# Kernel tuning notes

Hardware: AMD Instinct MI355X
Metric: run time of the kernel (lower is better)

Reference implementation:

```python
import jax, jax.numpy as jnp
import numpy as np

N = 100000      # nodes
E = 1600000     # edges
G = 1000        # graphs in the batch
D_IN, D_H, D_OUT = 128, 128, 64


def setup_inputs() -> dict:
    key = jax.random.key(0)
    ks = jax.random.split(key, 8)
    x = jax.random.normal(ks[0], (N, D_IN), jnp.float32)
    edge_index = jax.random.randint(ks[1], (2, E), 0, N, dtype=jnp.int32)
    batch = jnp.sort(jax.random.randint(ks[2], (N,), 0, G, dtype=jnp.int32))
    s_in = 1.0 / np.sqrt(D_IN)
    s_h = 1.0 / np.sqrt(D_H)
    return {
        "x": x,
        "edge_index": edge_index,
        "batch": batch,
        "W_emb": jax.random.normal(ks[3], (D_IN, D_H), jnp.float32) * s_in,
        "b_emb": jnp.zeros((D_H,), jnp.float32),
        "W1": jax.random.normal(ks[4], (D_H, D_H), jnp.float32) * s_h,
        "b1": jnp.zeros((D_H,), jnp.float32),
        "W2": jax.random.normal(ks[5], (D_H, D_H), jnp.float32) * s_h,
        "b2": jnp.zeros((D_H,), jnp.float32),
        "W3": jax.random.normal(ks[6], (D_H, D_OUT), jnp.float32) * s_h,
        "b3": jnp.zeros((D_OUT,), jnp.float32),
    }


def reference(x, edge_index, batch, W_emb, b_emb, W1, b1, W2, b2, W3, b3):
    # Eval mode: dropout is identity.
    n = x.shape[0]
    src, dst = edge_index[0], edge_index[1]
    # GCN symmetric normalization with self-loops (Kipf & Welling).
    deg = jax.ops.segment_sum(jnp.ones(src.shape[0], x.dtype), dst, num_segments=n) + 1.0
    dis = jax.lax.rsqrt(deg)                 # deg^{-1/2}, [N]
    edge_norm = dis[src] * dis[dst]          # [E]
    self_norm = dis * dis                    # self-loop weight = 1/deg, [N]

    def gcn_conv(h, W, b):
        h = h @ W                                         # [N, d_out]
        agg = jax.ops.segment_sum(h[src] * edge_norm[:, None], dst, num_segments=n)
        return agg + h * self_norm[:, None] + b

    h = x @ W_emb + b_emb
    h = jax.nn.relu(gcn_conv(h, W1, b1))
    h = jax.nn.relu(gcn_conv(h, W2, b2))
    h = gcn_conv(h, W3, b3)
    # global_add_pool over graph ids
    return jax.ops.segment_sum(h, batch, num_segments=G)
```

## Files before the change

### kernel.cpp

```cpp
#include <hip/hip_runtime.h>
#include <hip/hip_bf16.h>

#define NN 100000
#define NE 1600000
#define NG 1000
#define SMAX 48

typedef unsigned short u16;
typedef unsigned int u32;
typedef u16 u16x8 __attribute__((ext_vector_type(8)));
typedef u32 u32x4 __attribute__((ext_vector_type(4)));
typedef float f32x4 __attribute__((ext_vector_type(4)));
typedef __attribute__((ext_vector_type(8))) short s16x8;
typedef __attribute__((ext_vector_type(4))) float facc4;

__device__ __forceinline__ float bf2f(u16 u) {
    union { u32 i; float f; } c; c.i = ((u32)u) << 16; return c.f;
}
__device__ __forceinline__ u16 f2bf(float f) {
    __hip_bfloat16 h = __float2bfloat16(f);
    union { __hip_bfloat16 h; u16 u; } c; c.h = h; return c.u;
}

__global__ __launch_bounds__(256) void detect_kernel(const u32* __restrict__ xr, int* __restrict__ flag) {
    __shared__ int cnt[256];
    int c = 0;
    for (int i = threadIdx.x; i < 4096; i += 256) {
        u32 e = (xr[i] >> 7) & 0xFFu;
        if (e >= 110u && e <= 135u) c++;
    }
    cnt[threadIdx.x] = c;
    __syncthreads();
    for (int o = 128; o > 0; o >>= 1) {
        if (threadIdx.x < o) cnt[threadIdx.x] += cnt[threadIdx.x + o];
        __syncthreads();
    }
    if (threadIdx.x == 0) flag[0] = (cnt[0] > 2048) ? 1 : 0;
}

#define MEGA_NB 12726
__global__ __launch_bounds__(256) void mega_prep(
    const void* __restrict__ x, const int* __restrict__ flag, u16* __restrict__ xb,
    const void* __restrict__ Wemb, const void* __restrict__ W1, const void* __restrict__ W2,
    const void* __restrict__ W3, u16* __restrict__ wembT, u16* __restrict__ w1T,
    u16* __restrict__ w2T, u16* __restrict__ w3T,
    const void* __restrict__ bemb, const void* __restrict__ b1, const void* __restrict__ b2,
    const void* __restrict__ b3, float* __restrict__ bembF, float* __restrict__ b1F,
    float* __restrict__ b2F, float* __restrict__ b3F,
    const int* __restrict__ ei, int* __restrict__ counts)
{
    int b = blockIdx.x, tid = threadIdx.x;
    int fl = flag[0];
    if (b < 6250) {
        if (fl) return;
        int c = b * 256 + tid;
        f32x4 a = reinterpret_cast<const f32x4*>(x)[c * 2];
        f32x4 d = reinterpret_cast<const f32x4*>(x)[c * 2 + 1];
        u16x8 o;
        #pragma unroll
        for (int j = 0; j < 4; ++j) { o[j] = f2bf(a[j]); o[4 + j] = f2bf(d[j]); }
        reinterpret_cast<u16x8*>(xb)[c] = o;
    } else if (b < 6474) {
        int o = (b - 6250) * 256 + tid;
        const void* src; u16* dst; int M; int ol;
        if (o < 16384)      { src = Wemb; dst = wembT; M = 128; ol = o; }
        else if (o < 32768) { src = W1;   dst = w1T;   M = 128; ol = o - 16384; }
        else if (o < 49152) { src = W2;   dst = w2T;   M = 128; ol = o - 32768; }
        else                { src = W3;   dst = w3T;   M = 64;  ol = o - 49152; }
        int n = ol >> 7, k = ol & 127;
        u16 v = fl ? reinterpret_cast<const u16*>(src)[k * M + n]
                   : f2bf(reinterpret_cast<const float*>(src)[k * M + n]);
        dst[ol] = v;
    } else if (b < 6476) {
        int i = (b - 6474) * 256 + tid;
        if (i >= 448) return;
        const void* src; float* dst; int il;
        if (i < 128)      { src = bemb; dst = bembF; il = i; }
        else if (i < 256) { src = b1;   dst = b1F;   il = i - 128; }
        else if (i < 384) { src = b2;   dst = b2F;   il = i - 256; }
        else              { src = b3;   dst = b3F;   il = i - 384; }
        dst[il] = fl ? bf2f(reinterpret_cast<const u16*>(src)[il])
                     : reinterpret_cast<const float*>(src)[il];
    } else {
        int e = (b - 6476) * 256 + tid;
        if (e < NE) atomicAdd(&counts[ei[NE + e]], 1);
    }
}

__global__ __launch_bounds__(256) void wfuse_kernel(const u16* __restrict__ w1T, const u16* __restrict__ wembT,
                                                    const float* __restrict__ bembF,
                                                    u16* __restrict__ WfT, float* __restrict__ bfW) {
    int b = blockIdx.x;
    if (b < 64) {
        int o = b * 256 + threadIdx.x;
        int n = o >> 7, k = o & 127;
        float acc = 0.f;
        #pragma unroll 4
        for (int j = 0; j < 128; ++j)
            acc += bf2f(w1T[n * 128 + j]) * bf2f(wembT[j * 128 + k]);
        WfT[o] = f2bf(acc);
    } else {
        int n = threadIdx.x;
        if (n < 128) {
            float acc = 0.f;
            for (int j = 0; j < 128; ++j)
                acc += bembF[j] * bf2f(w1T[n * 128 + j]);
            bfW[n] = acc;
        }
    }
}

__global__ __launch_bounds__(256) void scan1_kernel(const int* __restrict__ counts, int* __restrict__ offs,
                                                    int* __restrict__ bsums, float* __restrict__ dis,
                                                    int* __restrict__ cursor) {
    __shared__ int sums[256];
    int tid = threadIdx.x;
    int base = blockIdx.x * 2048 + tid * 8;
    int local[8];
    int s = 0;
    #pragma unroll
    for (int i = 0; i < 8; ++i) {
        int v = 0;
        if (base + i < NN) {
            v = counts[base + i];
            dis[base + i] = rsqrtf((float)v + 1.0f);
            cursor[base + i] = 0;
        }
        local[i] = s; s += v;
    }
    sums[tid] = s;
    __syncthreads();
    for (int o = 1; o < 256; o <<= 1) {
        int v = (tid >= o) ? sums[tid - o] : 0;
        __syncthreads();
        sums[tid] += v;
        __syncthreads();
    }
    int excl = sums[tid] - s;
    #pragma unroll
    for (int i = 0; i < 8; ++i)
        if (base + i < NN) offs[base + i] = excl + local[i];
    if (tid == 255) bsums[blockIdx.x] = sums[255];
}

__global__ __launch_bounds__(256) void scan3_kernel(int* __restrict__ offs, const int* __restrict__ bsums) {
    __shared__ int addv;
    int i = blockIdx.x * 256 + threadIdx.x;
    int bucket = blockIdx.x >> 3;
    if (threadIdx.x == 0) {
        int s = 0;
        for (int k = 0; k < bucket; ++k) s += bsums[k];
        addv = s;
    }
    __syncthreads();
    if (i < NN) offs[i] += addv;
}

__global__ __launch_bounds__(256) void scatter_kernel(const int* __restrict__ ei, const int* __restrict__ offs,
                                                      int* __restrict__ cursor, const float* __restrict__ dis,
                                                      int2* __restrict__ edges) {
    int e = blockIdx.x * 256 + threadIdx.x;
    if (e < NE) {
        int s = ei[e], d = ei[NE + e];
        int pos = offs[d] + atomicAdd(&cursor[d], 1);
        int2 pk;
        pk.x = s;
        pk.y = __float_as_int(dis[s] * dis[d]);
        edges[pos] = pk;
    }
}

__global__ __launch_bounds__(256) void gemm_emb(const u16* __restrict__ xb, const u16* __restrict__ xraw,
                                                const int* __restrict__ flag, const u16* __restrict__ WfT,
                                                const float* __restrict__ bfW, u16* __restrict__ Hout) {
    __shared__ u16 sW[128 * 136];
    int tid = threadIdx.x;
    const u16* A = flag[0] ? xraw : xb;
    for (int c = tid; c < 128 * 16; c += 256) {
        int n = c >> 4, kc = (c & 15) << 3;
        *reinterpret_cast<u16x8*>(sW + n * 136 + kc) = reinterpret_cast<const u16x8*>(WfT)[c];
    }
    __syncthreads();
    int wv = tid >> 6, lane = tid & 63;
    int m = lane & 15, quad = lane >> 4;
    int r0 = blockIdx.x * 64 + wv * 16;
    int ar = r0 + m; if (ar >= NN) ar = NN - 1;
    facc4 acc[8];
    #pragma unroll
    for (int t = 0; t < 8; ++t) acc[t] = (facc4){0.f, 0.f, 0.f, 0.f};
    const u16* arow = A + (size_t)ar * 128 + quad * 8;
    #pragma unroll
    for (int k0 = 0; k0 < 128; k0 += 32) {
        s16x8 a = *reinterpret_cast<const s16x8*>(arow + k0);
        #pragma unroll
        for (int t = 0; t < 8; ++t) {
            s16x8 bfr = *reinterpret_cast<const s16x8*>(sW + (t * 16 + m) * 136 + k0 + quad * 8);
            acc[t] = __builtin_amdgcn_mfma_f32_16x16x32_bf16(a, bfr, acc[t], 0, 0, 0);
        }
    }
    #pragma unroll
    for (int t = 0; t < 8; ++t) {
        int col = t * 16 + m;
        float bv = bfW[col];
        #pragma unroll
        for (int r = 0; r < 4; ++r) {
            int orow = r0 + quad * 4 + r;
            if (orow < NN)
                Hout[(size_t)orow * 128 + col] = f2bf(acc[t][r] + bv);
        }
    }
}

template <int MOUT>
__global__ __launch_bounds__(256) void fused_agg_gemm(const u16* __restrict__ T, const int* __restrict__ offs,
                                                      const int* __restrict__ counts, const float* __restrict__ dis,
                                                      const int2* __restrict__ edges, const float* __restrict__ aggbias,
                                                      const u16* __restrict__ Wt, u16* __restrict__ Hout) {
    constexpr int LDW = 136;
    __shared__ u16 sW[MOUT * LDW];
    __shared__ u16 sA[64 * LDW];
    int tid = threadIdx.x;
    for (int c = tid; c < MOUT * 16; c += 256) {
        int n = c >> 4, kc = (c & 15) << 3;
        *reinterpret_cast<u16x8*>(sW + n * LDW + kc) = reinterpret_cast<const u16x8*>(Wt)[c];
    }

    int lane = tid & 15, grp = tid >> 4;
    const u32x4* T4 = reinterpret_cast<const u32x4*>(T);
    for (int i = 0; i < 4; ++i) {
        int nl = grp * 4 + i;
        int n = blockIdx.x * 64 + nl;
        bool valid = n < NN;
        int nc = valid ? n : NN - 1;
        float di = dis[nc];
        float sn = di * di;
        u32x4 ts = T4[(size_t)nc * 16 + lane];
        float acc[8];
        #pragma unroll
        for (int q = 0; q < 4; ++q) {
            acc[2 * q]     = bf2f((u16)(ts[q] & 0xffffu)) * sn + aggbias[lane * 8 + 2 * q];
            acc[2 * q + 1] = bf2f((u16)(ts[q] >> 16))     * sn + aggbias[lane * 8 + 2 * q + 1];
        }
        int st = offs[nc], cnt = valid ? counts[nc] : 0;
        int j = 0;
        for (; j + 4 <= cnt; j += 4) {
            int2 e0 = edges[st + j];
            int2 e1 = edges[st + j + 1];
            int2 e2 = edges[st + j + 2];
            int2 e3 = edges[st + j + 3];
            u32x4 g0 = T4[(size_t)e0.x * 16 + lane];
            u32x4 g1 = T4[(size_t)e1.x * 16 + lane];
            u32x4 g2 = T4[(size_t)e2.x * 16 + lane];
            u32x4 g3 = T4[(size_t)e3.x * 16 + lane];
            float w0 = __int_as_float(e0.y), w1 = __int_as_float(e1.y);
            float w2 = __int_as_float(e2.y), w3 = __int_as_float(e3.y);
            #pragma unroll
            for (int q = 0; q < 4; ++q) {
                acc[2 * q]     += bf2f((u16)(g0[q] & 0xffffu)) * w0;
                acc[2 * q + 1] += bf2f((u16)(g0[q] >> 16))     * w0;
                acc[2 * q]     += bf2f((u16)(g1[q] & 0xffffu)) * w1;
                acc[2 * q + 1] += bf2f((u16)(g1[q] >> 16))     * w1;
                acc[2 * q]     += bf2f((u16)(g2[q] & 0xffffu)) * w2;
                acc[2 * q + 1] += bf2f((u16)(g2[q] >> 16))     * w2;
                acc[2 * q]     += bf2f((u16)(g3[q] & 0xffffu)) * w3;
                acc[2 * q + 1] += bf2f((u16)(g3[q] >> 16))     * w3;
            }
        }
        for (; j < cnt; ++j) {
            int2 e = edges[st + j];
            u32x4 g = T4[(size_t)e.x * 16 + lane];
            float w = __int_as_float(e.y);
            #pragma unroll
            for (int q = 0; q < 4; ++q) {
                acc[2 * q]     += bf2f((u16)(g[q] & 0xffffu)) * w;
                acc[2 * q + 1] += bf2f((u16)(g[q] >> 16))     * w;
            }
        }
        u16x8 pk;
        #pragma unroll
        for (int q = 0; q < 4; ++q) {
            pk[2 * q]     = f2bf(fmaxf(acc[2 * q], 0.0f));
            pk[2 * q + 1] = f2bf(fmaxf(acc[2 * q + 1], 0.0f));
        }
        *reinterpret_cast<u16x8*>(sA + nl * LDW + lane * 8) = pk;
    }
    __syncthreads();

    int wv = tid >> 6, l64 = tid & 63;
    int m = l64 & 15, quad = l64 >> 4;
    int r0 = blockIdx.x * 64 + wv * 16;
    constexpr int NT = MOUT / 16;
    facc4 gacc[NT];
    #pragma unroll
    for (int t = 0; t < NT; ++t) gacc[t] = (facc4){0.f, 0.f, 0.f, 0.f};
    #pragma unroll
    for (int k0 = 0; k0 < 128; k0 += 32) {
        s16x8 a = *reinterpret_cast<const s16x8*>(sA + (wv * 16 + m) * LDW + k0 + quad * 8);
        #pragma unroll
        for (int t = 0; t < NT; ++t) {
            s16x8 bfr = *reinterpret_cast<const s16x8*>(sW + (t * 16 + m) * LDW + k0 + quad * 8);
            gacc[t] = __builtin_amdgcn_mfma_f32_16x16x32_bf16(a, bfr, gacc[t], 0, 0, 0);
        }
    }
    #pragma unroll
    for (int t = 0; t < NT; ++t) {
        int col = t * 16 + m;
        #pragma unroll
        for (int r = 0; r < 4; ++r) {
            int orow = r0 + quad * 4 + r;
            if (orow < NN)
                Hout[(size_t)orow * MOUT + col] = f2bf(gacc[t][r]);
        }
    }
}

__global__ __launch_bounds__(256) void agg_pool_kernel(const u16* __restrict__ T, const int* __restrict__ offs,
                                                       const int* __restrict__ counts, const float* __restrict__ dis,
                                                       const int2* __restrict__ edges, const float* __restrict__ bias,
                                                       const int* __restrict__ batch, float* __restrict__ outF) {
    __shared__ float accG[SMAX * 64];
    __shared__ int sg0;
    int tid = threadIdx.x;
    for (int i = tid; i < SMAX * 64; i += 256) accG[i] = 0.0f;
    if (tid == 0) sg0 = batch[blockIdx.x * 32];
    __syncthreads();
    int g0 = sg0;
    int lane = tid & 7;
    int n = blockIdx.x * 32 + (tid >> 3);

    const u32x4* T4 = reinterpret_cast<const u32x4*>(T);
    float di = dis[n];
    float sn = di * di;
    u32x4 ts = T4[(size_t)n * 8 + lane];
    float acc[8];
    #pragma unroll
    for (int q = 0; q < 4; ++q) {
        acc[2 * q]     = bf2f((u16)(ts[q] & 0xffffu)) * sn + bias[lane * 8 + 2 * q];
        acc[2 * q + 1] = bf2f((u16)(ts[q] >> 16))     * sn + bias[lane * 8 + 2 * q + 1];
    }
    int st = offs[n], cnt = counts[n];
    int j = 0;
    for (; j + 4 <= cnt; j += 4) {
        int2 e0 = edges[st + j];
        int2 e1 = edges[st + j + 1];
        int2 e2 = edges[st + j + 2];
        int2 e3 = edges[st + j + 3];
        u32x4 g0v = T4[(size_t)e0.x * 8 + lane];
        u32x4 g1v = T4[(size_t)e1.x * 8 + lane];
        u32x4 g2v = T4[(size_t)e2.x * 8 + lane];
        u32x4 g3v = T4[(size_t)e3.x * 8 + lane];
        float w0 = __int_as_float(e0.y), w1 = __int_as_float(e1.y);
        float w2 = __int_as_float(e2.y), w3 = __int_as_float(e3.y);
        #pragma unroll
        for (int q = 0; q < 4; ++q) {
            acc[2 * q]     += bf2f((u16)(g0v[q] & 0xffffu)) * w0;
            acc[2 * q + 1] += bf2f((u16)(g0v[q] >> 16))     * w0;
            acc[2 * q]     += bf2f((u16)(g1v[q] & 0xffffu)) * w1;
            acc[2 * q + 1] += bf2f((u16)(g1v[q] >> 16))     * w1;
            acc[2 * q]     += bf2f((u16)(g2v[q] & 0xffffu)) * w2;
            acc[2 * q + 1] += bf2f((u16)(g2v[q] >> 16))     * w2;
            acc[2 * q]     += bf2f((u16)(g3v[q] & 0xffffu)) * w3;
            acc[2 * q + 1] += bf2f((u16)(g3v[q] >> 16))     * w3;
        }
    }
    for (; j < cnt; ++j) {
        int2 e = edges[st + j];
        u32x4 g = T4[(size_t)e.x * 8 + lane];
        float w = __int_as_float(e.y);
        #pragma unroll
        for (int q = 0; q < 4; ++q) {
            acc[2 * q]     += bf2f((u16)(g[q] & 0xffffu)) * w;
            acc[2 * q + 1] += bf2f((u16)(g[q] >> 16))     * w;
        }
    }

    int s = batch[n] - g0;
    if (s >= 0 && s < SMAX) {
        #pragma unroll
        for (int q = 0; q < 8; ++q)
            atomicAdd(&accG[s * 64 + lane * 8 + q], acc[q]);
    } else {
        #pragma unroll
        for (int q = 0; q < 8; ++q)
            atomicAdd(&outF[(size_t)(g0 + s) * 64 + lane * 8 + q], acc[q]);
    }
    __syncthreads();
    int gend = batch[blockIdx.x * 32 + 31];
    int span = gend - g0 + 1;
    if (span > SMAX) span = SMAX;
    for (int i = tid; i < span * 64; i += 256)
        atomicAdd(&outF[(size_t)g0 * 64 + i], accG[i]);
}

__global__ __launch_bounds__(256) void out_cvt_kernel(const float* __restrict__ outF, void* __restrict__ out,
                                                      const int* __restrict__ flag) {
    int i = blockIdx.x * 256 + threadIdx.x;
    if (i < NG * 64) {
        float v = outF[i];
        if (flag[0]) reinterpret_cast<u16*>(out)[i] = f2bf(v);
        else         reinterpret_cast<float*>(out)[i] = v;
    }
}

extern "C" void kernel_launch(void* const* d_in, const int* in_sizes, int n_in,
                              void* d_out, int out_size, void* d_ws, size_t ws_size,
                              hipStream_t stream) {
    const void* x     = d_in[0];
    const int* ei     = (const int*)d_in[1];
    const int* batch  = (const int*)d_in[2];
    const void* W_emb = d_in[3];
    const void* b_emb = d_in[4];
    const void* W1    = d_in[5];
    const void* b1    = d_in[6];
    const void* W2    = d_in[7];
    const void* b2    = d_in[8];
    const void* W3    = d_in[9];
    const void* b3    = d_in[10];

    char* p = (char*)d_ws;
    auto alloc = [&](size_t bytes) { void* r = p; p += (bytes + 255) & ~(size_t)255; return r; };
    int*   flag   = (int*)alloc(256);
    int*   counts = (int*)alloc(NN * 4);
    int*   cursor = (int*)alloc(NN * 4);
    int*   offs   = (int*)alloc(NN * 4);
    float* dis    = (float*)alloc(NN * 4);
    int*   bsums  = (int*)alloc(256 * 4);
    int2*  edges  = (int2*)alloc((size_t)NE * 8);
    u16*   wembT  = (u16*)alloc(128 * 128 * 2);
    u16*   w1T    = (u16*)alloc(128 * 128 * 2);
    u16*   w2T    = (u16*)alloc(128 * 128 * 2);
    u16*   w3T    = (u16*)alloc(64 * 128 * 2);
    u16*   WfT    = (u16*)alloc(128 * 128 * 2);
    float* bembF  = (float*)alloc(128 * 4);
    float* b1F    = (float*)alloc(128 * 4);
    float* b2F    = (float*)alloc(128 * 4);
    float* b3F    = (float*)alloc(64 * 4);
    float* bfW    = (float*)alloc(128 * 4);
    float* outF   = (float*)alloc((size_t)NG * 64 * 4);
    u16*   hA     = (u16*)alloc((size_t)(NN + 64) * 128 * 2);
    u16*   hB     = (u16*)alloc((size_t)(NN + 64) * 128 * 2);

    hipMemsetAsync(counts, 0, NN * 4, stream);
    hipMemsetAsync(outF, 0, (size_t)NG * 64 * 4, stream);

    const int SB = (NN + 2047) / 2048;
    const int NB = (NN + 255) / 256;
    const int GB = (NN + 63) / 64;
    const int EB = (NE + 255) / 256;

    detect_kernel<<<1, 256, 0, stream>>>((const u32*)x, flag);
    mega_prep<<<MEGA_NB, 256, 0, stream>>>(x, flag, hB, W_emb, W1, W2, W3, wembT, w1T, w2T, w3T,
                                           b_emb, b1, b2, b3, bembF, b1F, b2F, b3F, ei, counts);
    wfuse_kernel<<<65, 256, 0, stream>>>(w1T, wembT, bembF, WfT, bfW);
    scan1_kernel<<<SB, 256, 0, stream>>>(counts, offs, bsums, dis, cursor);
    scan3_kernel<<<NB, 256, 0, stream>>>(offs, bsums);
    scatter_kernel<<<EB, 256, 0, stream>>>(ei, offs, cursor, dis, edges);
    gemm_emb<<<GB, 256, 0, stream>>>(hB, (const u16*)x, flag, WfT, bfW, hA);
    fused_agg_gemm<128><<<GB, 256, 0, stream>>>(hA, offs, counts, dis, edges, b1F, w2T, hB);
    fused_agg_gemm<64><<<GB, 256, 0, stream>>>(hB, offs, counts, dis, edges, b2F, w3T, hA);
    agg_pool_kernel<<<NN / 32, 256, 0, stream>>>(hA, offs, counts, dis, edges, b3F, batch, outF);
    out_cvt_kernel<<<(NG * 64 + 255) / 256, 256, 0, stream>>>(outF, d_out, flag);
}
```

Measured before the change: 515.0 us.

## Record edge rank during counting and aggregate directly into MFMA A-fragments

The degree-counting atomic now stores each edge's rank within its destination bucket. The scatter pass then places edges without a second atomic pass, and the cursor array and its reset go away. The fused aggregation+GEMM kernel is restructured so each lane aggregates the exact features it needs as an MFMA A operand (16 nodes per wave, 4 column chunks per lane). This removes the LDS staging buffer and one round trip through shared memory. In exchange, register pressure rises (32 accumulators plus 8 gathered vectors per lane), the gather unroll drops from 4 to 2 edges, and the rank scratch buffer is aliased onto hA.

```diff
diff --git a/kernel.cpp b/kernel.cpp
--- a/kernel.cpp
+++ b/kernel.cpp
@@ -47,7 +47,7 @@
     const void* __restrict__ bemb, const void* __restrict__ b1, const void* __restrict__ b2,
     const void* __restrict__ b3, float* __restrict__ bembF, float* __restrict__ b1F,
     float* __restrict__ b2F, float* __restrict__ b3F,
-    const int* __restrict__ ei, int* __restrict__ counts)
+    const int* __restrict__ ei, int* __restrict__ counts, int* __restrict__ erank)
 {
     int b = blockIdx.x, tid = threadIdx.x;
     int fl = flag[0];
@@ -83,7 +83,10 @@
                      : reinterpret_cast<const float*>(src)[il];
     } else {
         int e = (b - 6476) * 256 + tid;
-        if (e < NE) atomicAdd(&counts[ei[NE + e]], 1);
+        if (e < NE) {
+            int d = ei[NE + e];
+            erank[e] = atomicAdd(&counts[d], 1);
+        }
     }
 }
 
@@ -111,8 +114,7 @@
 }
 
 __global__ __launch_bounds__(256) void scan1_kernel(const int* __restrict__ counts, int* __restrict__ offs,
-                                                    int* __restrict__ bsums, float* __restrict__ dis,
-                                                    int* __restrict__ cursor) {
+                                                    int* __restrict__ bsums, float* __restrict__ dis) {
     __shared__ int sums[256];
     int tid = threadIdx.x;
     int base = blockIdx.x * 2048 + tid * 8;
@@ -124,7 +126,6 @@
         if (base + i < NN) {
             v = counts[base + i];
             dis[base + i] = rsqrtf((float)v + 1.0f);
-            cursor[base + i] = 0;
         }
         local[i] = s; s += v;
     }
@@ -157,12 +158,12 @@
 }
 
 __global__ __launch_bounds__(256) void scatter_kernel(const int* __restrict__ ei, const int* __restrict__ offs,
-                                                      int* __restrict__ cursor, const float* __restrict__ dis,
+                                                      const int* __restrict__ erank, const float* __restrict__ dis,
                                                       int2* __restrict__ edges) {
     int e = blockIdx.x * 256 + threadIdx.x;
     if (e < NE) {
         int s = ei[e], d = ei[NE + e];
-        int pos = offs[d] + atomicAdd(&cursor[d], 1);
+        int pos = offs[d] + erank[e];
         int2 pk;
         pk.x = s;
         pk.y = __float_as_int(dis[s] * dis[d]);
@@ -218,90 +219,90 @@
                                                       const u16* __restrict__ Wt, u16* __restrict__ Hout) {
     constexpr int LDW = 136;
     __shared__ u16 sW[MOUT * LDW];
-    __shared__ u16 sA[64 * LDW];
     int tid = threadIdx.x;
     for (int c = tid; c < MOUT * 16; c += 256) {
         int n = c >> 4, kc = (c & 15) << 3;
         *reinterpret_cast<u16x8*>(sW + n * LDW + kc) = reinterpret_cast<const u16x8*>(Wt)[c];
     }
 
-    int lane = tid & 15, grp = tid >> 4;
+    int wv = tid >> 6, lane = tid & 63;
+    int m = lane & 15, quad = lane >> 4;
+    int n = blockIdx.x * 64 + wv * 16 + m;
+    bool valid = n < NN;
+    int nc = valid ? n : NN - 1;
     const u32x4* T4 = reinterpret_cast<const u32x4*>(T);
-    for (int i = 0; i < 4; ++i) {
-        int nl = grp * 4 + i;
-        int n = blockIdx.x * 64 + nl;
-        bool valid = n < NN;
-        int nc = valid ? n : NN - 1;
-        float di = dis[nc];
-        float sn = di * di;
-        u32x4 ts = T4[(size_t)nc * 16 + lane];
-        float acc[8];
+
+    float di = dis[nc];
+    float sn = di * di;
+    float acc[4][8];
+    #pragma unroll
+    for (int c = 0; c < 4; ++c) {
+        u32x4 ts = T4[(size_t)nc * 16 + quad + 4 * c];
         #pragma unroll
         for (int q = 0; q < 4; ++q) {
-            acc[2 * q]     = bf2f((u16)(ts[q] & 0xffffu)) * sn + aggbias[lane * 8 + 2 * q];
-            acc[2 * q + 1] = bf2f((u16)(ts[q] >> 16))     * sn + aggbias[lane * 8 + 2 * q + 1];
-        }
-        int st = offs[nc], cnt = valid ? counts[nc] : 0;
-        int j = 0;
-        for (; j + 4 <= cnt; j += 4) {
-            int2 e0 = edges[st + j];
-            int2 e1 = edges[st + j + 1];
-            int2 e2 = edges[st + j + 2];
-            int2 e3 = edges[st + j + 3];
-            u32x4 g0 = T4[(size_t)e0.x * 16 + lane];
-            u32x4 g1 = T4[(size_t)e1.x * 16 + lane];
-            u32x4 g2 = T4[(size_t)e2.x * 16 + lane];
-            u32x4 g3 = T4[(size_t)e3.x * 16 + lane];
-            float w0 = __int_as_float(e0.y), w1 = __int_as_float(e1.y);
-            float w2 = __int_as_float(e2.y), w3 = __int_as_float(e3.y);
+            int f = c * 32 + quad * 8 + 2 * q;
+            acc[c][2 * q]     = bf2f((u16)(ts[q] & 0xffffu)) * sn + aggbias[f];
+            acc[c][2 * q + 1] = bf2f((u16)(ts[q] >> 16))     * sn + aggbias[f + 1];
+        }
+    }
+    int st = offs[nc], cnt = valid ? counts[nc] : 0;
+    int j = 0;
+    for (; j + 2 <= cnt; j += 2) {
+        int2 e0 = edges[st + j];
+        int2 e1 = edges[st + j + 1];
+        u32x4 g0[4], g1[4];
+        #pragma unroll
+        for (int c = 0; c < 4; ++c) g0[c] = T4[(size_t)e0.x * 16 + quad + 4 * c];
+        #pragma unroll
+        for (int c = 0; c < 4; ++c) g1[c] = T4[(size_t)e1.x * 16 + quad + 4 * c];
+        float w0 = __int_as_float(e0.y), w1 = __int_as_float(e1.y);
+        #pragma unroll
+        for (int c = 0; c < 4; ++c)
             #pragma unroll
             for (int q = 0; q < 4; ++q) {
-                acc[2 * q]     += bf2f((u16)(g0[q] & 0xffffu)) * w0;
-                acc[2 * q + 1] += bf2f((u16)(g0[q] >> 16))     * w0;
-                acc[2 * q]     += bf2f((u16)(g1[q] & 0xffffu)) * w1;
-                acc[2 * q + 1] += bf2f((u16)(g1[q] >> 16))     * w1;
-                acc[2 * q]     += bf2f((u16)(g2[q] & 0xffffu)) * w2;
-                acc[2 * q + 1] += bf2f((u16)(g2[q] >> 16))     * w2;
-                acc[2 * q]     += bf2f((u16)(g3[q] & 0xffffu)) * w3;
-                acc[2 * q + 1] += bf2f((u16)(g3[q] >> 16))     * w3;
+                acc[c][2 * q]     += bf2f((u16)(g0[c][q] & 0xffffu)) * w0;
+                acc[c][2 * q + 1] += bf2f((u16)(g0[c][q] >> 16))     * w0;
+                acc[c][2 * q]     += bf2f((u16)(g1[c][q] & 0xffffu)) * w1;
+                acc[c][2 * q + 1] += bf2f((u16)(g1[c][q] >> 16))     * w1;
             }
-        }
-        for (; j < cnt; ++j) {
-            int2 e = edges[st + j];
-            u32x4 g = T4[(size_t)e.x * 16 + lane];
-            float w = __int_as_float(e.y);
+    }
+    for (; j < cnt; ++j) {
+        int2 e = edges[st + j];
+        u32x4 g[4];
+        #pragma unroll
+        for (int c = 0; c < 4; ++c) g[c] = T4[(size_t)e.x * 16 + quad + 4 * c];
+        float w = __int_as_float(e.y);
+        #pragma unroll
+        for (int c = 0; c < 4; ++c)
             #pragma unroll
             for (int q = 0; q < 4; ++q) {
-                acc[2 * q]     += bf2f((u16)(g[q] & 0xffffu)) * w;
-                acc[2 * q + 1] += bf2f((u16)(g[q] >> 16))     * w;
+                acc[c][2 * q]     += bf2f((u16)(g[c][q] & 0xffffu)) * w;
+                acc[c][2 * q + 1] += bf2f((u16)(g[c][q] >> 16))     * w;
             }
-        }
-        u16x8 pk;
-        #pragma unroll
-        for (int q = 0; q < 4; ++q) {
-            pk[2 * q]     = f2bf(fmaxf(acc[2 * q], 0.0f));
-            pk[2 * q + 1] = f2bf(fmaxf(acc[2 * q + 1], 0.0f));
-        }
-        *reinterpret_cast<u16x8*>(sA + nl * LDW + lane * 8) = pk;
-    }
-    __syncthreads();
-
-    int wv = tid >> 6, l64 = tid & 63;
-    int m = l64 & 15, quad = l64 >> 4;
-    int r0 = blockIdx.x * 64 + wv * 16;
+    }
+
+    s16x8 afrag[4];
+    #pragma unroll
+    for (int c = 0; c < 4; ++c)
+        #pragma unroll
+        for (int i = 0; i < 8; ++i)
+            afrag[c][i] = (short)f2bf(fmaxf(acc[c][i], 0.0f));
+
+    __syncthreads();
+
     constexpr int NT = MOUT / 16;
     facc4 gacc[NT];
     #pragma unroll
     for (int t = 0; t < NT; ++t) gacc[t] = (facc4){0.f, 0.f, 0.f, 0.f};
     #pragma unroll
-    for (int k0 = 0; k0 < 128; k0 += 32) {
-        s16x8 a = *reinterpret_cast<const s16x8*>(sA + (wv * 16 + m) * LDW + k0 + quad * 8);
+    for (int c = 0; c < 4; ++c) {
         #pragma unroll
         for (int t = 0; t < NT; ++t) {
-            s16x8 bfr = *reinterpret_cast<const s16x8*>(sW + (t * 16 + m) * LDW + k0 + quad * 8);
-            gacc[t] = __builtin_amdgcn_mfma_f32_16x16x32_bf16(a, bfr, gacc[t], 0, 0, 0);
-        }
-    }
+            s16x8 bfr = *reinterpret_cast<const s16x8*>(sW + (t * 16 + m) * LDW + 32 * c + quad * 8);
+            gacc[t] = __builtin_amdgcn_mfma_f32_16x16x32_bf16(afrag[c], bfr, gacc[t], 0, 0, 0);
+        }
+    }
+    int r0 = blockIdx.x * 64 + wv * 16;
     #pragma unroll
     for (int t = 0; t < NT; ++t) {
         int col = t * 16 + m;
@@ -421,7 +422,6 @@
     auto alloc = [&](size_t bytes) { void* r = p; p += (bytes + 255) & ~(size_t)255; return r; };
     int*   flag   = (int*)alloc(256);
     int*   counts = (int*)alloc(NN * 4);
-    int*   cursor = (int*)alloc(NN * 4);
     int*   offs   = (int*)alloc(NN * 4);
     float* dis    = (float*)alloc(NN * 4);
     int*   bsums  = (int*)alloc(256 * 4);
@@ -439,6 +439,7 @@
     float* outF   = (float*)alloc((size_t)NG * 64 * 4);
     u16*   hA     = (u16*)alloc((size_t)(NN + 64) * 128 * 2);
     u16*   hB     = (u16*)alloc((size_t)(NN + 64) * 128 * 2);
+    int*   erank  = (int*)hA;
 
     hipMemsetAsync(counts, 0, NN * 4, stream);
     hipMemsetAsync(outF, 0, (size_t)NG * 64 * 4, stream);
@@ -450,11 +451,11 @@
 
     detect_kernel<<<1, 256, 0, stream>>>((const u32*)x, flag);
     mega_prep<<<MEGA_NB, 256, 0, stream>>>(x, flag, hB, W_emb, W1, W2, W3, wembT, w1T, w2T, w3T,
-                                           b_emb, b1, b2, b3, bembF, b1F, b2F, b3F, ei, counts);
+                                           b_emb, b1, b2, b3, bembF, b1F, b2F, b3F, ei, counts, erank);
     wfuse_kernel<<<65, 256, 0, stream>>>(w1T, wembT, bembF, WfT, bfW);
-    scan1_kernel<<<SB, 256, 0, stream>>>(counts, offs, bsums, dis, cursor);
+    scan1_kernel<<<SB, 256, 0, stream>>>(counts, offs, bsums, dis);
     scan3_kernel<<<NB, 256, 0, stream>>>(offs, bsums);
-    scatter_kernel<<<EB, 256, 0, stream>>>(ei, offs, cursor, dis, edges);
+    scatter_kernel<<<EB, 256, 0, stream>>>(ei, offs, erank, dis, edges);
     gemm_emb<<<GB, 256, 0, stream>>>(hB, (const u16*)x, flag, WfT, bfW, hA);
     fused_agg_gemm<128><<<GB, 256, 0, stream>>>(hA, offs, counts, dis, edges, b1F, w2T, hB);
     fused_agg_gemm<64><<<GB, 256, 0, stream>>>(hB, offs, counts, dis, edges, b2F, w3T, hA);
```

Measured after the change: 482.1 us. 6.4% less time.
